# Kernel optimization log

Hardware: AMD Instinct MI355X
Metric: run time of the kernel (lower is better)

## Reference

```python
import jax, jax.numpy as jnp
import numpy as np
import math

B, T, C, H = 4, 4096, 1024, 16
D = C // H

def setup_inputs() -> dict:
    key = jax.random.key(0)
    k1, k2, k3, k4, k5 = jax.random.split(key, 5)
    s = 1.0 / math.sqrt(C)
    return {
        "x": jax.random.normal(k1, (B, T, C), dtype=jnp.float32),
        "W_qkv": jax.random.normal(k2, (C, 3 * C), dtype=jnp.float32) * s,
        "b_qkv": jax.random.normal(k3, (3 * C,), dtype=jnp.float32) * 0.01,
        "W_out": jax.random.normal(k4, (C, C), dtype=jnp.float32) * s,
        "b_out": jax.random.normal(k5, (C,), dtype=jnp.float32) * 0.01,
    }

def reference(x, W_qkv, b_qkv, W_out, b_out):
    qkv = x @ W_qkv + b_qkv                      # (B,T,3C)
    q, k, v = jnp.split(qkv, 3, axis=2)
    q = q.reshape(B, T, H, D)
    k = k.reshape(B, T, H, D)
    v = v.reshape(B, T, H, D)
    # attention over the HEAD axis per (B,T): scores (B,T,H,H)
    att = jnp.einsum('bthd,btgd->bthg', q, k) / math.sqrt(D)
    att = jax.nn.softmax(att, axis=-1)
    out = jnp.einsum('bthg,btgd->bthd', att, v)  # (B,T,H,D)
    out = out.reshape(B, T, C)
    return out @ W_out + b_out
```

## Files before the change

### kernel.cpp

```cpp
#include <hip/hip_runtime.h>
#include <cstdint>
#include <cstddef>

constexpr int Bc = 4;
constexpr int Tc = 4096;
constexpr int Cc = 1024;
constexpr int Hc = 16;
constexpr int Dc = 64;
constexpr int Mc = Bc * Tc;
constexpr int N1c = 3 * Cc;
constexpr int Kc = Cc;
constexpr int KBc = Kc / 32;

typedef __bf16 bf16x8 __attribute__((ext_vector_type(8)));
typedef float  f32x4  __attribute__((ext_vector_type(4)));
typedef __attribute__((address_space(1))) uint32_t gu32;
typedef __attribute__((address_space(3))) uint32_t lu32;

__device__ __forceinline__ float bf2f(unsigned short u) {
    return __uint_as_float(((unsigned)u) << 16);
}
__device__ __forceinline__ unsigned short f2bf(float f) {
    unsigned u = __float_as_uint(f);
    u += 0x7FFF + ((u >> 16) & 1);
    return (unsigned short)(u >> 16);
}

__device__ __forceinline__ void load_lds16(const void* g, void* l) {
    __builtin_amdgcn_global_load_lds((gu32*)(uintptr_t)g, (lu32*)(uintptr_t)l, 16, 0, 0);
}


__global__ __launch_bounds__(256) void prep_kernel(
    const float* __restrict__ x,    unsigned short* __restrict__ Ap,
    const float* __restrict__ Wqkv, unsigned short* __restrict__ Wqkp,
    const float* __restrict__ Wout, unsigned short* __restrict__ Wop) {
    __shared__ float tile[32][33];
    const int bid = blockIdx.x;
    const int tid = threadIdx.x;

    if (bid < 8192) {
        const int w = tid >> 6, lane = tid & 63;
        const int t = bid * 4 + w;
        const int mb = t >> 5, kb = t & 31;
        const int r = lane >> 2, c = lane & 3;
        const float* src = x + (size_t)(mb * 16 + r) * Kc + kb * 32 + c * 8;
        float4 f0 = *(const float4*)src;
        float4 f1 = *(const float4*)(src + 4);
        unsigned short u[8];
        u[0] = f2bf(f0.x); u[1] = f2bf(f0.y); u[2] = f2bf(f0.z); u[3] = f2bf(f0.w);
        u[4] = f2bf(f1.x); u[5] = f2bf(f1.y); u[6] = f2bf(f1.z); u[7] = f2bf(f1.w);
        *(uint4*)(Ap + (size_t)t * 512 + (c * 16 + r) * 8) = *(uint4*)u;
        return;
    }

    const float* W; unsigned short* Bp; int N; int b2;
    if (bid < 8192 + 3072) { W = Wqkv; Bp = Wqkp; N = 3072; b2 = bid - 8192; }
    else                   { W = Wout; Bp = Wop;  N = 1024; b2 = bid - 11264; }
    const int NT = N >> 5;
    const int n0 = (b2 % NT) * 32, k0 = (b2 / NT) * 32;
    const int tx = tid & 31, ty = tid >> 5;
    for (int i = ty; i < 32; i += 8)
        tile[i][tx] = W[(size_t)(k0 + i) * N + n0 + tx];
    __syncthreads();
    const int t = tid;
    const int h = t >> 7, rr = t & 127, lane = rr >> 1, half = rr & 1;
    const int fq = lane >> 4, fn = lane & 15;
    unsigned short u[4];
    #pragma unroll
    for (int j = 0; j < 4; ++j)
        u[j] = f2bf(tile[fq * 8 + half * 4 + j][h * 16 + fn]);
    size_t tileIdx = (size_t)((n0 >> 4) + h) * (Kc >> 5) + (k0 >> 5);
    *(uint2*)(Bp + tileIdx * 512 + lane * 8 + half * 4) = *(uint2*)u;
}

template <bool OUT_BF16>
__global__ __launch_bounds__(256, 4) void lds_gemm_kernel(
    const unsigned short* __restrict__ Ap,
    const unsigned short* __restrict__ Bp,
    const float* __restrict__ bias,
    void* __restrict__ Cout,
    int M, int N, int K, int NB) {
    __shared__ unsigned short sA[16 * 512];
    __shared__ unsigned short sB[16 * 512];
    const int KB = K >> 5;
    const int MB = M >> 7;
    const int id   = blockIdx.x;
    const int xcd  = id & 7;
    const int per  = id >> 3;
    const int MSTR = MB >> 3;
    const int byl  = per & 7;
    const int bx   = (per >> 3) % NB;
    const int pass = per / (8 * NB);
    const int by   = xcd * MSTR + pass * 8 + byl;

    const int w    = threadIdx.x >> 6;
    const int lane = threadIdx.x & 63;
    const int m0 = by * 128;
    const int n0 = bx * 128;
    const int wm = (w >> 1) * 64;
    const int wn = (w & 1) * 64;

    const unsigned short* gA[4];
    const unsigned short* gB[4];
    unsigned short* lA[4];
    unsigned short* lB[4];
    #pragma unroll
    for (int i = 0; i < 4; ++i) {
        const int t  = w * 4 + i;
        const int mt = t >> 1, s = t & 1;
        gA[i] = Ap + ((size_t)(by * 8 + mt) * KB + s) * 512 + lane * 8;
        gB[i] = Bp + ((size_t)(bx * 8 + mt) * KB + s) * 512 + lane * 8;
        lA[i] = sA + t * 512;
        lB[i] = sB + t * 512;
    }

    const unsigned short* aP = sA + (wm >> 4) * 2 * 512 + lane * 8;
    const unsigned short* bP = sB + (wn >> 4) * 2 * 512 + lane * 8;

    const f32x4 zero4 = {0.f, 0.f, 0.f, 0.f};
    f32x4 acc[4][4];
    #pragma unroll
    for (int i = 0; i < 4; ++i)
        #pragma unroll
        for (int j = 0; j < 4; ++j) acc[i][j] = zero4;

    const int NIT = K >> 6;
    #pragma unroll 1
    for (int jt = 0; jt < NIT; ++jt) {
        #pragma unroll
        for (int i = 0; i < 4; ++i) {
            load_lds16(gA[i], lA[i]);
            load_lds16(gB[i], lB[i]);
        }
        #pragma unroll
        for (int i = 0; i < 4; ++i) { gA[i] += 1024; gB[i] += 1024; }
        __syncthreads();

        #pragma unroll
        for (int kk = 0; kk < 2; ++kk) {
            bf16x8 af[4], bfr[4];
            #pragma unroll
            for (int mi = 0; mi < 4; ++mi)
                af[mi]  = *(const bf16x8*)(aP + (mi * 2 + kk) * 512);
            #pragma unroll
            for (int ni = 0; ni < 4; ++ni)
                bfr[ni] = *(const bf16x8*)(bP + (ni * 2 + kk) * 512);
            #pragma unroll
            for (int mi = 0; mi < 4; ++mi)
                #pragma unroll
                for (int ni = 0; ni < 4; ++ni)
                    acc[mi][ni] = __builtin_amdgcn_mfma_f32_16x16x32_bf16(
                        af[mi], bfr[ni], acc[mi][ni], 0, 0, 0);
        }
        __syncthreads();
    }

    const int fr = lane & 15;
    const int fq = lane >> 4;
    #pragma unroll
    for (int mi = 0; mi < 4; ++mi) {
        #pragma unroll
        for (int ni = 0; ni < 4; ++ni) {
            int row = m0 + wm + mi * 16 + fq * 4;
            int col = n0 + wn + ni * 16 + fr;
            float bb = bias[col];
            #pragma unroll
            for (int r = 0; r < 4; ++r) {
                float v = acc[mi][ni][r] + bb;
                if (OUT_BF16)
                    ((unsigned short*)Cout)[(size_t)(row + r) * N + col] = f2bf(v);
                else
                    ((float*)Cout)[(size_t)(row + r) * N + col] = v;
            }
        }
    }
}

__global__ __launch_bounds__(256) void attn_mfma_kernel(
    const unsigned short* __restrict__ qkv,
    unsigned short* __restrict__ attP) {
    __shared__ char smem[4 * 4480];
    const int w    = threadIdx.x >> 6;
    const int lane = threadIdx.x & 63;
    const int m    = lane & 15;
    const int q    = lane >> 4;
    const int row  = blockIdx.x * 4 + w;
    unsigned short* sVt = (unsigned short*)(smem + w * 4480);
    float*          sP  = (float*)(smem + w * 4480 + 3200);

    const unsigned short* src = qkv + (size_t)row * 3072;

    bf16x8 aq0 = *(const bf16x8*)(src + m * 64 + q * 8);
    bf16x8 aq1 = *(const bf16x8*)(src + m * 64 + 32 + q * 8);
    bf16x8 bk0 = *(const bf16x8*)(src + 1024 + m * 64 + q * 8);
    bf16x8 bk1 = *(const bf16x8*)(src + 1024 + m * 64 + 32 + q * 8);

    #pragma unroll
    for (int t = 0; t < 2; ++t) {
        int G = t * 64 + lane;
        int g = G >> 3, p = G & 7;
        uint4 vv = *(const uint4*)(src + 2048 + G * 8);
        const unsigned short* vs = (const unsigned short*)&vv;
        #pragma unroll
        for (int i = 0; i < 8; ++i)
            sVt[200 * p + 24 * i + g] = vs[i];
    }

    f32x4 s = {0.f, 0.f, 0.f, 0.f};
    s = __builtin_amdgcn_mfma_f32_16x16x32_bf16(aq0, bk0, s, 0, 0, 0);
    s = __builtin_amdgcn_mfma_f32_16x16x32_bf16(aq1, bk1, s, 0, 0, 0);

    #pragma unroll
    for (int r = 0; r < 4; ++r) {
        float t0 = s[r] * 0.125f;
        float mx = t0;
        mx = fmaxf(mx, __shfl_xor(mx, 1));
        mx = fmaxf(mx, __shfl_xor(mx, 2));
        mx = fmaxf(mx, __shfl_xor(mx, 4));
        mx = fmaxf(mx, __shfl_xor(mx, 8));
        float e = __expf(t0 - mx);
        float su = e;
        su += __shfl_xor(su, 1);
        su += __shfl_xor(su, 2);
        su += __shfl_xor(su, 4);
        su += __shfl_xor(su, 8);
        sP[(q * 4 + r) * 20 + m] = e / su;
    }
    __syncthreads();

    const float* pr = sP + m * 20 + (q & 1) * 8;
    float4 pf0 = *(const float4*)(pr);
    float4 pf1 = *(const float4*)(pr + 4);
    const bool act = (q < 2);
    union { unsigned short u[8]; bf16x8 b; } pa;
    pa.u[0] = act ? f2bf(pf0.x) : 0;
    pa.u[1] = act ? f2bf(pf0.y) : 0;
    pa.u[2] = act ? f2bf(pf0.z) : 0;
    pa.u[3] = act ? f2bf(pf0.w) : 0;
    pa.u[4] = act ? f2bf(pf1.x) : 0;
    pa.u[5] = act ? f2bf(pf1.y) : 0;
    pa.u[6] = act ? f2bf(pf1.z) : 0;
    pa.u[7] = act ? f2bf(pf1.w) : 0;

    float o4[4][4];
    #pragma unroll
    for (int c4 = 0; c4 < 4; ++c4) {
        const int d = c4 * 16 + m;
        bf16x8 vf = *(const bf16x8*)(sVt + d * 24 + (d >> 3) * 8 + (q & 1) * 8);
        f32x4 o = {0.f, 0.f, 0.f, 0.f};
        o = __builtin_amdgcn_mfma_f32_16x16x32_bf16(pa.b, vf, o, 0, 0, 0);
        #pragma unroll
        for (int r = 0; r < 4; ++r) o4[c4][r] = o[r];
    }
    __syncthreads();

    unsigned short* sO = sVt;
    #pragma unroll
    for (int c4 = 0; c4 < 4; ++c4) {
        #pragma unroll
        for (int r = 0; r < 4; ++r) {
            int col = (q * 4 + r) * 64 + c4 * 16 + m;
            sO[col + ((col >> 6) << 3)] = f2bf(o4[c4][r]);
        }
    }
    __syncthreads();

    const size_t tileBase = (size_t)(row >> 4) * 32 * 512;
    const int fr_tok = row & 15;
    #pragma unroll
    for (int t = 0; t < 2; ++t) {
        int j = t * 64 + lane;
        uint4 val = *(const uint4*)(sO + j * 8 + ((j >> 3) << 3));
        *(uint4*)(attP + tileBase + (size_t)(j >> 2) * 512
                  + ((j & 3) * 16 + fr_tok) * 8) = val;
    }
}

extern "C" void kernel_launch(void* const* d_in, const int* in_sizes, int n_in,
                              void* d_out, int out_size, void* d_ws, size_t ws_size,
                              hipStream_t stream) {
    const float* x    = (const float*)d_in[0];
    const float* Wqkv = (const float*)d_in[1];
    const float* bqkv = (const float*)d_in[2];
    const float* Wout = (const float*)d_in[3];
    const float* bout = (const float*)d_in[4];
    float* out = (float*)d_out;

    char* ws = (char*)d_ws;
    unsigned short* xp   = (unsigned short*)ws;                 ws += (size_t)Mc * Kc * 2;
    unsigned short* Wqkp = (unsigned short*)ws;                 ws += (size_t)N1c * Kc * 2;
    unsigned short* Wop  = (unsigned short*)ws;                 ws += (size_t)Cc * Kc * 2;
    unsigned short* qkv  = (unsigned short*)ws;
    unsigned short* attP = xp;

    prep_kernel<<<8192 + 3072 + 1024, 256, 0, stream>>>(x, xp, Wqkv, Wqkp, Wout, Wop);

    for (int p = 0; p < 3; ++p) {
        const unsigned short* Bp_p = Wqkp + (size_t)p * 64 * KBc * 512;
        lds_gemm_kernel<true><<<8 * (Mc / 128), 256, 0, stream>>>(
            xp, Bp_p, bqkv + p * 1024, qkv + p * 1024, Mc, N1c, Kc, 8);
    }

    attn_mfma_kernel<<<Mc / 4, 256, 0, stream>>>(qkv, attP);

    lds_gemm_kernel<false><<<(Cc / 128) * (Mc / 128), 256, 0, stream>>>(
        attP, Wop, bout, out, Mc, Cc, Kc, Cc / 128);
}
```

Baseline: 309.0 us.

## Fuse all stages into one cooperative persistent kernel with grid syncs

Replaces the sequence of kernel launches (prep, three QKV GEMM slices, attention, output GEMM) with one cooperative kernel of 1024 blocks that loops over each stage's work items, separated by grid-wide barriers. The goal is to remove launch gaps and tail effects between stages. The QKV GEMM becomes a single launch over all N instead of three slices, and the old multi-kernel path stays as a fallback. The risks are the cost of the grid syncs, a fixed grid of 1024 that must all be co-resident, and a larger shared-memory footprint for stages that needed less.

```diff
diff --git a/kernel.cpp b/kernel.cpp
--- a/kernel.cpp
+++ b/kernel.cpp
@@ -1,6 +1,9 @@
 #include <hip/hip_runtime.h>
+#include <hip/hip_cooperative_groups.h>
 #include <cstdint>
 #include <cstddef>
+
+namespace cg = cooperative_groups;
 
 constexpr int Bc = 4;
 constexpr int Tc = 4096;
@@ -17,9 +20,6 @@
 typedef __attribute__((address_space(1))) uint32_t gu32;
 typedef __attribute__((address_space(3))) uint32_t lu32;
 
-__device__ __forceinline__ float bf2f(unsigned short u) {
-    return __uint_as_float(((unsigned)u) << 16);
-}
 __device__ __forceinline__ unsigned short f2bf(float f) {
     unsigned u = __float_as_uint(f);
     u += 0x7FFF + ((u >> 16) & 1);
@@ -31,14 +31,12 @@
 }
 
 
-__global__ __launch_bounds__(256) void prep_kernel(
+__device__ __forceinline__ void prep_body(
+    int bid, int tid,
     const float* __restrict__ x,    unsigned short* __restrict__ Ap,
     const float* __restrict__ Wqkv, unsigned short* __restrict__ Wqkp,
-    const float* __restrict__ Wout, unsigned short* __restrict__ Wop) {
-    __shared__ float tile[32][33];
-    const int bid = blockIdx.x;
-    const int tid = threadIdx.x;
-
+    const float* __restrict__ Wout, unsigned short* __restrict__ Wop,
+    char* smemc) {
     if (bid < 8192) {
         const int w = tid >> 6, lane = tid & 63;
         const int t = bid * 4 + w;
@@ -53,10 +51,11 @@
         *(uint4*)(Ap + (size_t)t * 512 + (c * 16 + r) * 8) = *(uint4*)u;
         return;
     }
-
+    float (*tile)[33] = (float(*)[33])smemc;
     const float* W; unsigned short* Bp; int N; int b2;
     if (bid < 8192 + 3072) { W = Wqkv; Bp = Wqkp; N = 3072; b2 = bid - 8192; }
     else                   { W = Wout; Bp = Wop;  N = 1024; b2 = bid - 11264; }
+    __syncthreads();
     const int NT = N >> 5;
     const int n0 = (b2 % NT) * 32, k0 = (b2 / NT) * 32;
     const int tx = tid & 31, ty = tid >> 5;
@@ -75,27 +74,25 @@
 }
 
 template <bool OUT_BF16>
-__global__ __launch_bounds__(256, 4) void lds_gemm_kernel(
+__device__ __forceinline__ void gemm_body(
+    int id, int tid,
     const unsigned short* __restrict__ Ap,
     const unsigned short* __restrict__ Bp,
     const float* __restrict__ bias,
     void* __restrict__ Cout,
-    int M, int N, int K, int NB) {
-    __shared__ unsigned short sA[16 * 512];
-    __shared__ unsigned short sB[16 * 512];
+    int M, int N, int K, int NB, char* smemc) {
+    unsigned short* sA = (unsigned short*)smemc;
+    unsigned short* sB = sA + 16 * 512;
     const int KB = K >> 5;
-    const int MB = M >> 7;
-    const int id   = blockIdx.x;
     const int xcd  = id & 7;
     const int per  = id >> 3;
-    const int MSTR = MB >> 3;
     const int byl  = per & 7;
     const int bx   = (per >> 3) % NB;
     const int pass = per / (8 * NB);
-    const int by   = xcd * MSTR + pass * 8 + byl;
-
-    const int w    = threadIdx.x >> 6;
-    const int lane = threadIdx.x & 63;
+    const int by   = xcd * ((M >> 7) >> 3) + pass * 8 + byl;
+
+    const int w    = tid >> 6;
+    const int lane = tid & 63;
     const int m0 = by * 128;
     const int n0 = bx * 128;
     const int wm = (w >> 1) * 64;
@@ -177,17 +174,17 @@
     }
 }
 
-__global__ __launch_bounds__(256) void attn_mfma_kernel(
+__device__ __forceinline__ void attn_body(
+    int vb, int tid,
     const unsigned short* __restrict__ qkv,
-    unsigned short* __restrict__ attP) {
-    __shared__ char smem[4 * 4480];
-    const int w    = threadIdx.x >> 6;
-    const int lane = threadIdx.x & 63;
+    unsigned short* __restrict__ attP, char* smemc) {
+    const int w    = tid >> 6;
+    const int lane = tid & 63;
     const int m    = lane & 15;
     const int q    = lane >> 4;
-    const int row  = blockIdx.x * 4 + w;
-    unsigned short* sVt = (unsigned short*)(smem + w * 4480);
-    float*          sP  = (float*)(smem + w * 4480 + 3200);
+    const int row  = vb * 4 + w;
+    unsigned short* sVt = (unsigned short*)(smemc + w * 4480);
+    float*          sP  = (float*)(smemc + w * 4480 + 3200);
 
     const unsigned short* src = qkv + (size_t)row * 3072;
 
@@ -277,6 +274,54 @@
     }
 }
 
+__global__ __launch_bounds__(256, 4) void mega_kernel(
+    const float* __restrict__ x,    unsigned short* __restrict__ xp,
+    const float* __restrict__ Wqkv, unsigned short* __restrict__ Wqkp,
+    const float* __restrict__ Wout, unsigned short* __restrict__ Wop,
+    const float* __restrict__ bqkv, unsigned short* __restrict__ qkv,
+    const float* __restrict__ bout, float* __restrict__ out) {
+    __shared__ __align__(16) char smem[32768];
+    cg::grid_group grid = cg::this_grid();
+    const int bid = blockIdx.x, tid = threadIdx.x;
+
+    for (int t = bid; t < 12288; t += 1024)
+        prep_body(t, tid, x, xp, Wqkv, Wqkp, Wout, Wop, smem);
+    grid.sync();
+    for (int t = bid; t < 3072; t += 1024)
+        gemm_body<true>(t, tid, xp, Wqkp, bqkv, qkv, Mc, N1c, Kc, N1c / 128, smem);
+    grid.sync();
+    for (int t = bid; t < 4096; t += 1024)
+        attn_body(t, tid, qkv, xp, smem);
+    grid.sync();
+    gemm_body<false>(bid, tid, xp, Wop, bout, out, Mc, Cc, Kc, Cc / 128, smem);
+}
+
+__global__ __launch_bounds__(256) void prep_kernel(
+    const float* __restrict__ x,    unsigned short* __restrict__ Ap,
+    const float* __restrict__ Wqkv, unsigned short* __restrict__ Wqkp,
+    const float* __restrict__ Wout, unsigned short* __restrict__ Wop) {
+    __shared__ __align__(16) char smem[4224];
+    prep_body(blockIdx.x, threadIdx.x, x, Ap, Wqkv, Wqkp, Wout, Wop, smem);
+}
+
+template <bool OUT_BF16>
+__global__ __launch_bounds__(256, 4) void lds_gemm_kernel(
+    const unsigned short* __restrict__ Ap,
+    const unsigned short* __restrict__ Bp,
+    const float* __restrict__ bias,
+    void* __restrict__ Cout,
+    int M, int N, int K, int NB) {
+    __shared__ __align__(16) char smem[32768];
+    gemm_body<OUT_BF16>(blockIdx.x, threadIdx.x, Ap, Bp, bias, Cout, M, N, K, NB, smem);
+}
+
+__global__ __launch_bounds__(256) void attn_mfma_kernel(
+    const unsigned short* __restrict__ qkv,
+    unsigned short* __restrict__ attP) {
+    __shared__ __align__(16) char smem[17920];
+    attn_body(blockIdx.x, threadIdx.x, qkv, attP, smem);
+}
+
 extern "C" void kernel_launch(void* const* d_in, const int* in_sizes, int n_in,
                               void* d_out, int out_size, void* d_ws, size_t ws_size,
                               hipStream_t stream) {
@@ -292,18 +337,28 @@
     unsigned short* Wqkp = (unsigned short*)ws;                 ws += (size_t)N1c * Kc * 2;
     unsigned short* Wop  = (unsigned short*)ws;                 ws += (size_t)Cc * Kc * 2;
     unsigned short* qkv  = (unsigned short*)ws;
-    unsigned short* attP = xp;
+
+    static int coop_ok = -1;
+    if (coop_ok != 0) {
+        void* args[] = {
+            (void*)&x,    (void*)&xp,
+            (void*)&Wqkv, (void*)&Wqkp,
+            (void*)&Wout, (void*)&Wop,
+            (void*)&bqkv, (void*)&qkv,
+            (void*)&bout, (void*)&out,
+        };
+        hipError_t e = hipLaunchCooperativeKernel(
+            reinterpret_cast<const void*>(mega_kernel),
+            dim3(1024), dim3(256), args, 0, stream);
+        if (e == hipSuccess) { coop_ok = 1; return; }
+        (void)hipGetLastError();
+        coop_ok = 0;
+    }
 
     prep_kernel<<<8192 + 3072 + 1024, 256, 0, stream>>>(x, xp, Wqkv, Wqkp, Wout, Wop);
-
-    for (int p = 0; p < 3; ++p) {
-        const unsigned short* Bp_p = Wqkp + (size_t)p * 64 * KBc * 512;
-        lds_gemm_kernel<true><<<8 * (Mc / 128), 256, 0, stream>>>(
-            xp, Bp_p, bqkv + p * 1024, qkv + p * 1024, Mc, N1c, Kc, 8);
-    }
-
-    attn_mfma_kernel<<<Mc / 4, 256, 0, stream>>>(qkv, attP);
-
+    lds_gemm_kernel<true><<<(N1c / 128) * (Mc / 128), 256, 0, stream>>>(
+        xp, Wqkp, bqkv, qkv, Mc, N1c, Kc, N1c / 128);
+    attn_mfma_kernel<<<Mc / 4, 256, 0, stream>>>(qkv, xp);
     lds_gemm_kernel<false><<<(Cc / 128) * (Mc / 128), 256, 0, stream>>>(
-        attP, Wop, bout, out, Mc, Cc, Kc, Cc / 128);
-}
+        xp, Wop, bout, out, Mc, Cc, Kc, Cc / 128);
+}
```

Result: faster. 287.5 us (-7.0%).

## Add 256x256 tile GEMM with 512 threads and double-buffered LDS

Applied to the files above, without the earlier changes.

Introduces a new GEMM kernel using 256x256 output tiles, 8 waves per block, 128 KB of dynamic LDS and a double-buffered global-to-LDS prefetch. It replaces both the three per-slice QKV GEMM launches (now a single launch over all 3072 columns) and the output projection GEMM, falling back to the old kernel if the large LDS attribute cannot be set. The larger tile raises data reuse per LDS byte and cuts launch count, at the cost of more registers and lower occupancy.

```diff
diff --git a/kernel.cpp b/kernel.cpp
--- a/kernel.cpp
+++ b/kernel.cpp
@@ -17,9 +17,6 @@
 typedef __attribute__((address_space(1))) uint32_t gu32;
 typedef __attribute__((address_space(3))) uint32_t lu32;
 
-__device__ __forceinline__ float bf2f(unsigned short u) {
-    return __uint_as_float(((unsigned)u) << 16);
-}
 __device__ __forceinline__ unsigned short f2bf(float f) {
     unsigned u = __float_as_uint(f);
     u += 0x7FFF + ((u >> 16) & 1);
@@ -72,6 +69,124 @@
         u[j] = f2bf(tile[fq * 8 + half * 4 + j][h * 16 + fn]);
     size_t tileIdx = (size_t)((n0 >> 4) + h) * (Kc >> 5) + (k0 >> 5);
     *(uint2*)(Bp + tileIdx * 512 + lane * 8 + half * 4) = *(uint2*)u;
+}
+
+template <bool OUT_BF16>
+__global__ __launch_bounds__(512, 2) void gemm256_kernel(
+    const unsigned short* __restrict__ Ap,
+    const unsigned short* __restrict__ Bp,
+    const float* __restrict__ bias,
+    void* __restrict__ Cout,
+    int M, int N, int K, int NB) {
+    extern __shared__ unsigned short sm[];
+    const int KB = K >> 5;
+    const int id  = blockIdx.x;
+    const int xcd = id & 7;
+    const int per = id >> 3;
+    const int MSTR = (M >> 8) >> 3;
+    const int byl  = per & 7;
+    const int bx   = (per >> 3) % NB;
+    const int pass = per / (8 * NB);
+    const int by   = xcd * MSTR + pass * 8 + byl;
+
+    const int w    = threadIdx.x >> 6;
+    const int lane = threadIdx.x & 63;
+    const int wm   = w >> 2;
+    const int wn   = w & 3;
+    constexpr int BUF = 64 * 512;
+
+    const bool isA = (w < 4);
+    const int  w4  = isA ? w : (w - 4);
+    const unsigned short* gS[8];
+    unsigned short* lS[8];
+    #pragma unroll
+    for (int i = 0; i < 8; ++i) {
+        const int t  = w4 * 8 + i;
+        const int mt = t >> 1, ks = t & 1;
+        const unsigned short* base = isA
+            ? Ap + ((size_t)(by * 16 + mt) * KB + ks) * 512
+            : Bp + ((size_t)(bx * 16 + mt) * KB + ks) * 512;
+        gS[i] = base + lane * 8;
+        lS[i] = sm + (isA ? 0 : 32 * 512) + t * 512;
+    }
+
+    const unsigned short* aR = sm + (wm * 8) * 2 * 512 + lane * 8;
+    const unsigned short* bR = sm + 32 * 512 + (wn * 4) * 2 * 512 + lane * 8;
+
+    const f32x4 zero4 = {0.f, 0.f, 0.f, 0.f};
+    f32x4 acc[8][4];
+    #pragma unroll
+    for (int i = 0; i < 8; ++i)
+        #pragma unroll
+        for (int j = 0; j < 4; ++j) acc[i][j] = zero4;
+
+    const int NST = K >> 6;
+    #pragma unroll
+    for (int i = 0; i < 8; ++i) load_lds16(gS[i], lS[i]);
+    __syncthreads();
+
+    #pragma unroll 1
+    for (int k = 0; k < NST; ++k) {
+        const int c = k & 1;
+        const unsigned short* aC = aR + c * BUF;
+        const unsigned short* bC = bR + c * BUF;
+
+        if (k + 1 < NST) {
+            const size_t o = (size_t)(k + 1) * 1024;
+            const int d = (c ^ 1) * BUF;
+            #pragma unroll
+            for (int i = 0; i < 8; ++i) load_lds16(gS[i] + o, lS[i] + d);
+        }
+
+        bf16x8 bfr[8];
+        #pragma unroll
+        for (int nt = 0; nt < 8; ++nt)
+            bfr[nt] = *(const bf16x8*)(bC + nt * 512);
+
+        #pragma unroll
+        for (int p = 0; p < 4; ++p) {
+            bf16x8 af[4];
+            #pragma unroll
+            for (int j = 0; j < 4; ++j)
+                af[j] = *(const bf16x8*)(aC + ((2 * p + (j >> 1)) * 2 + (j & 1)) * 512);
+            __builtin_amdgcn_sched_barrier(0);
+            __builtin_amdgcn_s_setprio(1);
+            #pragma unroll
+            for (int ml = 0; ml < 2; ++ml)
+                #pragma unroll
+                for (int ni = 0; ni < 4; ++ni) {
+                    acc[2 * p + ml][ni] = __builtin_amdgcn_mfma_f32_16x16x32_bf16(
+                        af[ml * 2 + 0], bfr[ni * 2 + 0], acc[2 * p + ml][ni], 0, 0, 0);
+                    acc[2 * p + ml][ni] = __builtin_amdgcn_mfma_f32_16x16x32_bf16(
+                        af[ml * 2 + 1], bfr[ni * 2 + 1], acc[2 * p + ml][ni], 0, 0, 0);
+                }
+            __builtin_amdgcn_s_setprio(0);
+            __builtin_amdgcn_sched_barrier(0);
+        }
+        __syncthreads();
+    }
+
+    const int fr = lane & 15;
+    const int fq = lane >> 4;
+    const int m0 = by * 256 + wm * 128;
+    const int n0 = bx * 256 + wn * 64;
+    #pragma unroll
+    for (int mi = 0; mi < 8; ++mi) {
+        #pragma unroll
+        for (int ni = 0; ni < 4; ++ni) {
+            int row = m0 + mi * 16 + fq * 4;
+            int col = n0 + ni * 16 + fr;
+            float bb = bias[col];
+            #pragma unroll
+            for (int r = 0; r < 4; ++r) {
+                float v = acc[mi][ni][r] + bb;
+                if (OUT_BF16)
+                    ((unsigned short*)Cout)[(size_t)(row + r) * N + col] = f2bf(v);
+                else
+                    ((float*)Cout)[(size_t)(row + r) * N + col] = v;
+            }
+        }
+    }
 }
 
 template <bool OUT_BF16>
@@ -292,18 +407,34 @@
     unsigned short* Wqkp = (unsigned short*)ws;                 ws += (size_t)N1c * Kc * 2;
     unsigned short* Wop  = (unsigned short*)ws;                 ws += (size_t)Cc * Kc * 2;
     unsigned short* qkv  = (unsigned short*)ws;
-    unsigned short* attP = xp;
+
+    constexpr int DYN_LDS = 2 * 64 * 512 * 2;
+    static int big_ok = -1;
+    if (big_ok < 0) {
+        hipError_t e1 = hipFuncSetAttribute(
+            reinterpret_cast<const void*>(gemm256_kernel<true>),
+            hipFuncAttributeMaxDynamicSharedMemorySize, DYN_LDS);
+        hipError_t e2 = hipFuncSetAttribute(
+            reinterpret_cast<const void*>(gemm256_kernel<false>),
+            hipFuncAttributeMaxDynamicSharedMemorySize, DYN_LDS);
+        big_ok = (e1 == hipSuccess && e2 == hipSuccess) ? 1 : 0;
+    }
 
     prep_kernel<<<8192 + 3072 + 1024, 256, 0, stream>>>(x, xp, Wqkv, Wqkp, Wout, Wop);
 
-    for (int p = 0; p < 3; ++p) {
-        const unsigned short* Bp_p = Wqkp + (size_t)p * 64 * KBc * 512;
-        lds_gemm_kernel<true><<<8 * (Mc / 128), 256, 0, stream>>>(
-            xp, Bp_p, bqkv + p * 1024, qkv + p * 1024, Mc, N1c, Kc, 8);
-    }
-
-    attn_mfma_kernel<<<Mc / 4, 256, 0, stream>>>(qkv, attP);
-
-    lds_gemm_kernel<false><<<(Cc / 128) * (Mc / 128), 256, 0, stream>>>(
-        attP, Wop, bout, out, Mc, Cc, Kc, Cc / 128);
-}
+    if (big_ok)
+        gemm256_kernel<true><<<(Mc / 256) * (N1c / 256), 512, DYN_LDS, stream>>>(
+            xp, Wqkp, bqkv, qkv, Mc, N1c, Kc, N1c / 256);
+    else
+        lds_gemm_kernel<true><<<(N1c / 128) * (Mc / 128), 256, 0, stream>>>(
+            xp, Wqkp, bqkv, qkv, Mc, N1c, Kc, N1c / 128);
+
+    attn_mfma_kernel<<<Mc / 4, 256, 0, stream>>>(qkv, xp);
+
+    if (big_ok)
+        gemm256_kernel<false><<<(Mc / 256) * (Cc / 256), 512, DYN_LDS, stream>>>(
+            xp, Wop, bout, out, Mc, Cc, Kc, Cc / 256);
+    else
+        lds_gemm_kernel<false><<<(Cc / 128) * (Mc / 128), 256, 0, stream>>>(
+            xp, Wop, bout, out, Mc, Cc, Kc, Cc / 128);
+}
```

Measured after the change: 291.4 us. 1.06x faster.
